# Optimization experiments

Measured on AMD Instinct MI355X. Metric: run time of the kernel, lower is better.

Reference implementation:

```python
import jax, jax.numpy as jnp
import numpy as np

NUM_TREES = 256
DEPTH = 6
TREE_DIM = 2
INPUT_DIM = 256
BATCH = 2048


def sparsemax(x, axis=0):
    # Euclidean projection onto the simplex along `axis`.
    x = jnp.moveaxis(x, axis, -1)
    z = jnp.flip(jnp.sort(x, axis=-1), axis=-1)           # descending
    cz = jnp.cumsum(z, axis=-1)
    k = jnp.arange(1, x.shape[-1] + 1, dtype=x.dtype)
    support = (1.0 + k * z) > cz                          # boolean support set
    k_sel = jnp.sum(support, axis=-1, keepdims=True)      # |S(z)|
    tau = (jnp.take_along_axis(cz, k_sel - 1, axis=-1) - 1.0) / k_sel.astype(x.dtype)
    out = jnp.maximum(x - tau, 0.0)
    return jnp.moveaxis(out, -1, axis)


def sparsemoid(x):
    return jnp.clip(0.5 * x + 0.5, 0.0, 1.0)


def make_bin_codes(depth):
    idx = np.arange(2 ** depth)
    offs = 2 ** np.arange(depth)
    bc = ((idx[None, :] // offs[:, None]) % 2).astype(np.float32)  # [depth, 2^depth]
    return jnp.asarray(np.stack([bc, 1.0 - bc], axis=-1))          # [depth, 2^depth, 2]


def setup_inputs() -> dict:
    key = jax.random.key(0)
    ks = jax.random.split(key, 5)
    return {
        "inputs": jax.random.normal(ks[0], (BATCH, INPUT_DIM), dtype=jnp.float32),
        "feature_selection_logits": jax.random.normal(ks[1], (INPUT_DIM, NUM_TREES, DEPTH), dtype=jnp.float32),
        "feature_thresholds": jax.random.normal(ks[2], (NUM_TREES, DEPTH), dtype=jnp.float32) * 0.5,
        "log_temperatures": jax.random.normal(ks[3], (NUM_TREES, DEPTH), dtype=jnp.float32) * 0.1,
        "response": jax.random.normal(ks[4], (NUM_TREES, TREE_DIM, 2 ** DEPTH), dtype=jnp.float32),
    }


def reference(inputs, feature_selection_logits, feature_thresholds, log_temperatures, response):
    bin_codes_1hot = make_bin_codes(DEPTH)                                  # [d, 2^d, 2]
    selectors = sparsemax(feature_selection_logits, axis=0)                 # [i, n, d]
    feature_values = jnp.einsum('bi,ind->bnd', inputs, selectors)           # [b, n, d]
    tl = (feature_values - feature_thresholds) * jnp.exp(-log_temperatures) # [b, n, d]
    threshold_logits = jnp.stack([-tl, tl], axis=-1)                        # [b, n, d, 2]
    bins = sparsemoid(threshold_logits)                                     # [b, n, d, 2]
    bin_matches = jnp.einsum('bnds,dcs->bndc', bins, bin_codes_1hot)        # [b, n, d, 2^d]
    response_weights = jnp.prod(bin_matches, axis=-2)                       # [b, n, 2^d]
    out = jnp.einsum('bnc,ntc->bnt', response_weights, response)            # [b, n, tree_dim]
    return out.reshape(out.shape[0], -1)                                    # [b, n*tree_dim]
```

## Files before the change

### kernel.cpp

```cpp
#include <hip/hip_runtime.h>
#include <hip/hip_fp16.h>
#include <math.h>

#define NUM_TREES 256
#define DEPTH 6
#define TREE_DIM 2
#define INPUT_DIM 256
#define BATCH 2048
#define NLEAF 64
#define NCOLS (NUM_TREES * DEPTH)
#define KDIM INPUT_DIM

typedef _Float16 half8 __attribute__((ext_vector_type(8)));
typedef float floatx4 __attribute__((ext_vector_type(4)));

__global__ __launch_bounds__(256) void sparsemax_bisect(
    const float* __restrict__ fsl,
    _Float16* __restrict__ selT)
{
    const int lane = threadIdx.x & 63;
    const int wave = threadIdx.x >> 6;
    const int col  = blockIdx.x * 4 + wave;
    const int n = col / 6;
    const int d = col - n * 6;

    float x[4];
#pragma unroll
    for (int j = 0; j < 4; ++j)
        x[j] = fsl[(j * 64 + lane) * NCOLS + col];

    float mx = fmaxf(fmaxf(x[0], x[1]), fmaxf(x[2], x[3]));
#pragma unroll
    for (int off = 32; off > 0; off >>= 1)
        mx = fmaxf(mx, __shfl_xor(mx, off));

    float lo = mx - 1.0f, hi = mx;
    for (int it = 0; it < 24; ++it) {
        const float mid = 0.5f * (lo + hi);
        float s = fmaxf(x[0] - mid, 0.0f) + fmaxf(x[1] - mid, 0.0f)
                + fmaxf(x[2] - mid, 0.0f) + fmaxf(x[3] - mid, 0.0f);
#pragma unroll
        for (int off = 32; off > 0; off >>= 1)
            s += __shfl_xor(s, off);
        if (s > 1.0f) lo = mid; else hi = mid;
    }
    const float tau = 0.5f * (lo + hi);

    _Float16* dst = selT + (n * 8 + d) * KDIM;
#pragma unroll
    for (int j = 0; j < 4; ++j)
        dst[j * 64 + lane] = (_Float16)fmaxf(x[j] - tau, 0.0f);
}

#define BM 128
#define BN 64
#define BK 32
#define FVS 68

__global__ __launch_bounds__(256) void odt_mfma_kernel(
    const float* __restrict__ inputs,
    const _Float16* __restrict__ selT,
    const float* __restrict__ thr,
    const float* __restrict__ logt,
    const float* __restrict__ resp,
    float* __restrict__ out)
{
    __shared__ _Float16 Asm[BM][BK];
    __shared__ _Float16 Bsm[BN][BK];
    __shared__ float    fvS[BM][FVS];
    __shared__ float    respS[8 * TREE_DIM * NLEAF];

    const int tid = threadIdx.x;
    const int b0 = blockIdx.x * BM;
    const int treeBase = blockIdx.y * 8;
    const int colBase  = blockIdx.y * BN;

    ((float4*)respS)[tid] = ((const float4*)(resp + treeBase * TREE_DIM * NLEAF))[tid];

    const int lane = tid & 63;
    const int w    = tid >> 6;
    const int wm   = w >> 1, wn = w & 1;
    const int l16  = lane & 15, quad = lane >> 4;

    floatx4 acc[4][2];
#pragma unroll
    for (int mt = 0; mt < 4; ++mt)
#pragma unroll
        for (int nt = 0; nt < 2; ++nt)
            acc[mt][nt] = (floatx4){0.f, 0.f, 0.f, 0.f};

    const int arow = tid >> 1, ach = tid & 1;
    const int bcol = tid >> 2, bkc = tid & 3;

    for (int k0 = 0; k0 < KDIM; k0 += BK) {
        __syncthreads();
        {
            const float4* g = (const float4*)(inputs + (b0 + arow) * KDIM + k0 + ach * 16);
            const float4 v0 = g[0], v1 = g[1], v2 = g[2], v3 = g[3];
            half8 h0, h1;
            h0[0] = (_Float16)v0.x; h0[1] = (_Float16)v0.y; h0[2] = (_Float16)v0.z; h0[3] = (_Float16)v0.w;
            h0[4] = (_Float16)v1.x; h0[5] = (_Float16)v1.y; h0[6] = (_Float16)v1.z; h0[7] = (_Float16)v1.w;
            h1[0] = (_Float16)v2.x; h1[1] = (_Float16)v2.y; h1[2] = (_Float16)v2.z; h1[3] = (_Float16)v2.w;
            h1[4] = (_Float16)v3.x; h1[5] = (_Float16)v3.y; h1[6] = (_Float16)v3.z; h1[7] = (_Float16)v3.w;
            *(half8*)&Asm[arow][ach * 16]     = h0;
            *(half8*)&Asm[arow][ach * 16 + 8] = h1;
        }
        {
            const half8 v = *(const half8*)(selT + (colBase + bcol) * KDIM + k0 + bkc * 8);
            *(half8*)&Bsm[bcol][bkc * 8] = v;
        }
        __syncthreads();

        half8 bfr0 = *(half8*)&Bsm[wn * 32 + l16][quad * 8];
        half8 bfr1 = *(half8*)&Bsm[wn * 32 + 16 + l16][quad * 8];
#pragma unroll
        for (int mt = 0; mt < 4; ++mt) {
            half8 afr = *(half8*)&Asm[wm * 64 + mt * 16 + l16][quad * 8];
            acc[mt][0] = __builtin_amdgcn_mfma_f32_16x16x32_f16(afr, bfr0, acc[mt][0], 0, 0, 0);
            acc[mt][1] = __builtin_amdgcn_mfma_f32_16x16x32_f16(afr, bfr1, acc[mt][1], 0, 0, 0);
        }
    }

#pragma unroll
    for (int mt = 0; mt < 4; ++mt)
#pragma unroll
        for (int nt = 0; nt < 2; ++nt)
#pragma unroll
            for (int r = 0; r < 4; ++r)
                fvS[wm * 64 + mt * 16 + quad * 4 + r][wn * 32 + nt * 16 + l16] = acc[mt][nt][r];
    __syncthreads();

#pragma unroll
    for (int p = 0; p < 4; ++p) {
        const int idx = tid + 256 * p;
        const int row = idx & 127;
        const int tl  = idx >> 7;
        const int n   = treeBase + tl;
        const float* f = &fvS[row][tl * 8];

        float sd[DEPTH];
#pragma unroll
        for (int d = 0; d < DEPTH; ++d) {
            const float tlg = (f[d] - thr[n * DEPTH + d]) * __expf(-logt[n * DEPTH + d]);
            sd[d] = fminf(fmaxf(0.5f + 0.5f * tlg, 0.0f), 1.0f);
        }
        float wv[NLEAF];
        wv[0] = 1.0f;
#pragma unroll
        for (int d = 0; d < DEPTH; ++d) {
            const int sz = 1 << d;
#pragma unroll
            for (int c2 = 0; c2 < NLEAF / 2; ++c2) {
                if (c2 < sz) {
                    const float t = wv[c2];
                    wv[c2]      = t * sd[d];
                    wv[c2 + sz] = t * (1.0f - sd[d]);
                }
            }
        }
        const float* r0 = &respS[tl * TREE_DIM * NLEAF];
        float o0 = 0.0f, o1 = 0.0f;
#pragma unroll
        for (int c2 = 0; c2 < NLEAF; ++c2) {
            o0 = fmaf(wv[c2], r0[c2], o0);
            o1 = fmaf(wv[c2], r0[NLEAF + c2], o1);
        }
        float2 o = {o0, o1};
        *(float2*)(out + (b0 + row) * (NUM_TREES * TREE_DIM) + n * TREE_DIM) = o;
    }
}

extern "C" void kernel_launch(void* const* d_in, const int* in_sizes, int n_in,
                              void* d_out, int out_size, void* d_ws, size_t ws_size,
                              hipStream_t stream) {
    const float* inputs = (const float*)d_in[0];
    const float* fsl    = (const float*)d_in[1];
    const float* thr    = (const float*)d_in[2];
    const float* logt   = (const float*)d_in[3];
    const float* resp   = (const float*)d_in[4];
    float* out = (float*)d_out;
    _Float16* selT = (_Float16*)d_ws;

    hipLaunchKernelGGL(sparsemax_bisect, dim3(NCOLS / 4), dim3(256), 0, stream, fsl, selT);
    hipLaunchKernelGGL(odt_mfma_kernel, dim3(BATCH / BM, (NUM_TREES * 8) / BN), dim3(256),
                       0, stream, inputs, selT, thr, logt, resp, out);
}
```

Measured before the change: 91.08 us.

## Fuse sparsemax into single ODT kernel with register-direct A loads

Merges the sparsemax bisection and the MFMA/tree evaluation into one kernel. Each block recomputes sparsemax for its 48 selector columns in LDS, and the two-kernel launch plus the workspace round trip go away. It also drops padded depth columns (48 instead of 64), loads A fragments straight from global into registers with prefetch instead of staging them in LDS, halves the bisection iterations to 12, and folds the last depth level into the response reduction. The risks are redundant sparsemax work across the 8 batch blocks, lower precision of tau, and a small 256-block grid at one block per CU.

```diff
diff --git a/kernel.cpp b/kernel.cpp
--- a/kernel.cpp
+++ b/kernel.cpp
@@ -11,146 +11,162 @@
 #define NCOLS (NUM_TREES * DEPTH)
 #define KDIM INPUT_DIM
 
+#define BM 256
+#define TPB 8
+#define BCOLS (TPB * DEPTH)
+#define BSLP 260
+#define FVP 53
+
 typedef _Float16 half8 __attribute__((ext_vector_type(8)));
 typedef float floatx4 __attribute__((ext_vector_type(4)));
 
-__global__ __launch_bounds__(256) void sparsemax_bisect(
+__global__ __launch_bounds__(512, 1) void odt_one_kernel(
+    const float* __restrict__ inputs,
     const float* __restrict__ fsl,
-    _Float16* __restrict__ selT)
-{
-    const int lane = threadIdx.x & 63;
-    const int wave = threadIdx.x >> 6;
-    const int col  = blockIdx.x * 4 + wave;
-    const int n = col / 6;
-    const int d = col - n * 6;
-
-    float x[4];
-#pragma unroll
-    for (int j = 0; j < 4; ++j)
-        x[j] = fsl[(j * 64 + lane) * NCOLS + col];
-
-    float mx = fmaxf(fmaxf(x[0], x[1]), fmaxf(x[2], x[3]));
-#pragma unroll
-    for (int off = 32; off > 0; off >>= 1)
-        mx = fmaxf(mx, __shfl_xor(mx, off));
-
-    float lo = mx - 1.0f, hi = mx;
-    for (int it = 0; it < 24; ++it) {
-        const float mid = 0.5f * (lo + hi);
-        float s = fmaxf(x[0] - mid, 0.0f) + fmaxf(x[1] - mid, 0.0f)
-                + fmaxf(x[2] - mid, 0.0f) + fmaxf(x[3] - mid, 0.0f);
-#pragma unroll
-        for (int off = 32; off > 0; off >>= 1)
-            s += __shfl_xor(s, off);
-        if (s > 1.0f) lo = mid; else hi = mid;
-    }
-    const float tau = 0.5f * (lo + hi);
-
-    _Float16* dst = selT + (n * 8 + d) * KDIM;
-#pragma unroll
-    for (int j = 0; j < 4; ++j)
-        dst[j * 64 + lane] = (_Float16)fmaxf(x[j] - tau, 0.0f);
-}
-
-#define BM 128
-#define BN 64
-#define BK 32
-#define FVS 68
-
-__global__ __launch_bounds__(256) void odt_mfma_kernel(
-    const float* __restrict__ inputs,
-    const _Float16* __restrict__ selT,
     const float* __restrict__ thr,
     const float* __restrict__ logt,
     const float* __restrict__ resp,
     float* __restrict__ out)
 {
-    __shared__ _Float16 Asm[BM][BK];
-    __shared__ _Float16 Bsm[BN][BK];
-    __shared__ float    fvS[BM][FVS];
-    __shared__ float    respS[8 * TREE_DIM * NLEAF];
-
-    const int tid = threadIdx.x;
-    const int b0 = blockIdx.x * BM;
-    const int treeBase = blockIdx.y * 8;
-    const int colBase  = blockIdx.y * BN;
-
-    ((float4*)respS)[tid] = ((const float4*)(resp + treeBase * TREE_DIM * NLEAF))[tid];
-
+    __shared__ _Float16 Bsl[BCOLS][BSLP];
+    __shared__ float    fv[BM][FVP];
+    __shared__ float    respS[TPB * TREE_DIM * NLEAF];
+    __shared__ float    thrS[BCOLS], etS[BCOLS];
+
+    const int tid  = threadIdx.x;
     const int lane = tid & 63;
     const int w    = tid >> 6;
-    const int wm   = w >> 1, wn = w & 1;
-    const int l16  = lane & 15, quad = lane >> 4;
-
-    floatx4 acc[4][2];
-#pragma unroll
-    for (int mt = 0; mt < 4; ++mt)
-#pragma unroll
-        for (int nt = 0; nt < 2; ++nt)
+    const int b0   = blockIdx.x * BM;
+    const int treeBase = blockIdx.y * TPB;
+    const int col0 = treeBase * DEPTH;
+
+    ((float2*)respS)[tid] = ((const float2*)(resp + treeBase * TREE_DIM * NLEAF))[tid];
+    if (tid < BCOLS) {
+        thrS[tid] = thr[col0 + tid];
+        etS[tid]  = __expf(-logt[col0 + tid]);
+    }
+
+    {
+        float x[6][4];
+        const float* base = fsl + col0 + w * 6;
+#pragma unroll
+        for (int j = 0; j < 4; ++j) {
+            const float* r = base + (j * 64 + lane) * NCOLS;
+            const float2 v0 = *(const float2*)(r);
+            const float2 v1 = *(const float2*)(r + 2);
+            const float2 v2 = *(const float2*)(r + 4);
+            x[0][j] = v0.x; x[1][j] = v0.y; x[2][j] = v1.x;
+            x[3][j] = v1.y; x[4][j] = v2.x; x[5][j] = v2.y;
+        }
+        float lo[6], hi[6];
+#pragma unroll
+        for (int c = 0; c < 6; ++c) {
+            float m = fmaxf(fmaxf(x[c][0], x[c][1]), fmaxf(x[c][2], x[c][3]));
+#pragma unroll
+            for (int off = 32; off > 0; off >>= 1)
+                m = fmaxf(m, __shfl_xor(m, off));
+            hi[c] = m; lo[c] = m - 1.0f;
+        }
+        for (int it = 0; it < 12; ++it) {
+            float s[6], mid[6];
+#pragma unroll
+            for (int c = 0; c < 6; ++c) {
+                mid[c] = 0.5f * (lo[c] + hi[c]);
+                s[c] = fmaxf(x[c][0] - mid[c], 0.f) + fmaxf(x[c][1] - mid[c], 0.f)
+                     + fmaxf(x[c][2] - mid[c], 0.f) + fmaxf(x[c][3] - mid[c], 0.f);
+            }
+#pragma unroll
+            for (int off = 32; off > 0; off >>= 1)
+#pragma unroll
+                for (int c = 0; c < 6; ++c)
+                    s[c] += __shfl_xor(s[c], off);
+#pragma unroll
+            for (int c = 0; c < 6; ++c) {
+                if (s[c] > 1.0f) lo[c] = mid[c]; else hi[c] = mid[c];
+            }
+        }
+#pragma unroll
+        for (int c = 0; c < 6; ++c) {
+            const float tau = 0.5f * (lo[c] + hi[c]);
+#pragma unroll
+            for (int j = 0; j < 4; ++j)
+                Bsl[w * 6 + c][j * 64 + lane] = (_Float16)fmaxf(x[c][j] - tau, 0.f);
+        }
+    }
+    __syncthreads();
+
+    const int l16 = lane & 15, quad = lane >> 4;
+    floatx4 acc[2][3];
+#pragma unroll
+    for (int mt = 0; mt < 2; ++mt)
+#pragma unroll
+        for (int nt = 0; nt < 3; ++nt)
             acc[mt][nt] = (floatx4){0.f, 0.f, 0.f, 0.f};
 
-    const int arow = tid >> 1, ach = tid & 1;
-    const int bcol = tid >> 2, bkc = tid & 3;
-
-    for (int k0 = 0; k0 < KDIM; k0 += BK) {
-        __syncthreads();
-        {
-            const float4* g = (const float4*)(inputs + (b0 + arow) * KDIM + k0 + ach * 16);
-            const float4 v0 = g[0], v1 = g[1], v2 = g[2], v3 = g[3];
-            half8 h0, h1;
-            h0[0] = (_Float16)v0.x; h0[1] = (_Float16)v0.y; h0[2] = (_Float16)v0.z; h0[3] = (_Float16)v0.w;
-            h0[4] = (_Float16)v1.x; h0[5] = (_Float16)v1.y; h0[6] = (_Float16)v1.z; h0[7] = (_Float16)v1.w;
-            h1[0] = (_Float16)v2.x; h1[1] = (_Float16)v2.y; h1[2] = (_Float16)v2.z; h1[3] = (_Float16)v2.w;
-            h1[4] = (_Float16)v3.x; h1[5] = (_Float16)v3.y; h1[6] = (_Float16)v3.z; h1[7] = (_Float16)v3.w;
-            *(half8*)&Asm[arow][ach * 16]     = h0;
-            *(half8*)&Asm[arow][ach * 16 + 8] = h1;
-        }
-        {
-            const half8 v = *(const half8*)(selT + (colBase + bcol) * KDIM + k0 + bkc * 8);
-            *(half8*)&Bsm[bcol][bkc * 8] = v;
-        }
-        __syncthreads();
-
-        half8 bfr0 = *(half8*)&Bsm[wn * 32 + l16][quad * 8];
-        half8 bfr1 = *(half8*)&Bsm[wn * 32 + 16 + l16][quad * 8];
-#pragma unroll
-        for (int mt = 0; mt < 4; ++mt) {
-            half8 afr = *(half8*)&Asm[wm * 64 + mt * 16 + l16][quad * 8];
-            acc[mt][0] = __builtin_amdgcn_mfma_f32_16x16x32_f16(afr, bfr0, acc[mt][0], 0, 0, 0);
-            acc[mt][1] = __builtin_amdgcn_mfma_f32_16x16x32_f16(afr, bfr1, acc[mt][1], 0, 0, 0);
-        }
-    }
-
-#pragma unroll
-    for (int mt = 0; mt < 4; ++mt)
-#pragma unroll
-        for (int nt = 0; nt < 2; ++nt)
+    const float* aBase = inputs + (b0 + 32 * w + l16) * KDIM + quad * 8;
+    float4 p[2][2];
+#pragma unroll
+    for (int mt = 0; mt < 2; ++mt) {
+        p[mt][0] = *(const float4*)(aBase + mt * 16 * KDIM);
+        p[mt][1] = *(const float4*)(aBase + mt * 16 * KDIM + 4);
+    }
+
+    for (int k0 = 0; k0 < KDIM; k0 += 32) {
+        half8 af[2];
+#pragma unroll
+        for (int mt = 0; mt < 2; ++mt) {
+            af[mt][0] = (_Float16)p[mt][0].x; af[mt][1] = (_Float16)p[mt][0].y;
+            af[mt][2] = (_Float16)p[mt][0].z; af[mt][3] = (_Float16)p[mt][0].w;
+            af[mt][4] = (_Float16)p[mt][1].x; af[mt][5] = (_Float16)p[mt][1].y;
+            af[mt][6] = (_Float16)p[mt][1].z; af[mt][7] = (_Float16)p[mt][1].w;
+        }
+        if (k0 + 32 < KDIM) {
+#pragma unroll
+            for (int mt = 0; mt < 2; ++mt) {
+                p[mt][0] = *(const float4*)(aBase + mt * 16 * KDIM + k0 + 32);
+                p[mt][1] = *(const float4*)(aBase + mt * 16 * KDIM + k0 + 36);
+            }
+        }
+        const half8 bf0 = *(const half8*)&Bsl[l16][k0 + quad * 8];
+        const half8 bf1 = *(const half8*)&Bsl[16 + l16][k0 + quad * 8];
+        const half8 bf2 = *(const half8*)&Bsl[32 + l16][k0 + quad * 8];
+        acc[0][0] = __builtin_amdgcn_mfma_f32_16x16x32_f16(af[0], bf0, acc[0][0], 0, 0, 0);
+        acc[0][1] = __builtin_amdgcn_mfma_f32_16x16x32_f16(af[0], bf1, acc[0][1], 0, 0, 0);
+        acc[0][2] = __builtin_amdgcn_mfma_f32_16x16x32_f16(af[0], bf2, acc[0][2], 0, 0, 0);
+        acc[1][0] = __builtin_amdgcn_mfma_f32_16x16x32_f16(af[1], bf0, acc[1][0], 0, 0, 0);
+        acc[1][1] = __builtin_amdgcn_mfma_f32_16x16x32_f16(af[1], bf1, acc[1][1], 0, 0, 0);
+        acc[1][2] = __builtin_amdgcn_mfma_f32_16x16x32_f16(af[1], bf2, acc[1][2], 0, 0, 0);
+    }
+
+#pragma unroll
+    for (int mt = 0; mt < 2; ++mt)
+#pragma unroll
+        for (int nt = 0; nt < 3; ++nt)
 #pragma unroll
             for (int r = 0; r < 4; ++r)
-                fvS[wm * 64 + mt * 16 + quad * 4 + r][wn * 32 + nt * 16 + l16] = acc[mt][nt][r];
+                fv[32 * w + 16 * mt + 4 * quad + r][16 * nt + l16] = acc[mt][nt][r];
     __syncthreads();
 
 #pragma unroll
-    for (int p = 0; p < 4; ++p) {
-        const int idx = tid + 256 * p;
-        const int row = idx & 127;
-        const int tl  = idx >> 7;
-        const int n   = treeBase + tl;
-        const float* f = &fvS[row][tl * 8];
+    for (int pp = 0; pp < 4; ++pp) {
+        const int idx = tid + 512 * pp;
+        const int row = idx & 255;
+        const int tl  = idx >> 8;
+        const float* f = &fv[row][tl * 6];
 
         float sd[DEPTH];
 #pragma unroll
         for (int d = 0; d < DEPTH; ++d) {
-            const float tlg = (f[d] - thr[n * DEPTH + d]) * __expf(-logt[n * DEPTH + d]);
+            const float tlg = (f[d] - thrS[tl * 6 + d]) * etS[tl * 6 + d];
             sd[d] = fminf(fmaxf(0.5f + 0.5f * tlg, 0.0f), 1.0f);
         }
-        float wv[NLEAF];
+        float wv[NLEAF / 2];
         wv[0] = 1.0f;
 #pragma unroll
-        for (int d = 0; d < DEPTH; ++d) {
+        for (int d = 0; d < 5; ++d) {
             const int sz = 1 << d;
 #pragma unroll
-            for (int c2 = 0; c2 < NLEAF / 2; ++c2) {
+            for (int c2 = 0; c2 < 16; ++c2) {
                 if (c2 < sz) {
                     const float t = wv[c2];
                     wv[c2]      = t * sd[d];
@@ -159,14 +175,20 @@
             }
         }
         const float* r0 = &respS[tl * TREE_DIM * NLEAF];
-        float o0 = 0.0f, o1 = 0.0f;
-#pragma unroll
-        for (int c2 = 0; c2 < NLEAF; ++c2) {
-            o0 = fmaf(wv[c2], r0[c2], o0);
-            o1 = fmaf(wv[c2], r0[NLEAF + c2], o1);
-        }
-        float2 o = {o0, o1};
-        *(float2*)(out + (b0 + row) * (NUM_TREES * TREE_DIM) + n * TREE_DIM) = o;
+        float a0 = 0.f, c0 = 0.f, a1 = 0.f, c1 = 0.f;
+#pragma unroll
+        for (int c2 = 0; c2 < 32; ++c2) {
+            a0 = fmaf(wv[c2], r0[c2], a0);
+            c0 = fmaf(wv[c2], r0[c2 + 32], c0);
+            a1 = fmaf(wv[c2], r0[NLEAF + c2], a1);
+            c1 = fmaf(wv[c2], r0[NLEAF + c2 + 32], c1);
+        }
+        const float s5 = sd[5], s5b = 1.0f - sd[5];
+        float2 o;
+        o.x = s5 * a0 + s5b * c0;
+        o.y = s5 * a1 + s5b * c1;
+        *(float2*)(out + (b0 + row) * (NUM_TREES * TREE_DIM)
+                   + (treeBase + tl) * TREE_DIM) = o;
     }
 }
 
@@ -179,9 +201,8 @@
     const float* logt   = (const float*)d_in[3];
     const float* resp   = (const float*)d_in[4];
     float* out = (float*)d_out;
-    _Float16* selT = (_Float16*)d_ws;
-
-    hipLaunchKernelGGL(sparsemax_bisect, dim3(NCOLS / 4), dim3(256), 0, stream, fsl, selT);
-    hipLaunchKernelGGL(odt_mfma_kernel, dim3(BATCH / BM, (NUM_TREES * 8) / BN), dim3(256),
-                       0, stream, inputs, selT, thr, logt, resp, out);
+    (void)d_ws; (void)ws_size;
+
+    hipLaunchKernelGGL(odt_one_kernel, dim3(BATCH / BM, NUM_TREES / TPB), dim3(512),
+                       0, stream, inputs, fsl, thr, logt, resp, out);
 }
```

Measured after the change: 91.30 us. About the same (+0.2%).
